# Kernel tuning notes

Measured on AMD Instinct MI355X. Metric: run time of the kernel, lower is better.

Reference implementation:

```python
import jax, jax.numpy as jnp
import numpy as np

E = 8          # num_experts
K = 2          # top_k
TEMP = 1.0     # router_temp
D = 1024       # model dim
H = 4 * D      # expert hidden dim
B, T = 2, 2048


def setup_inputs() -> dict:
    key = jax.random.key(0)
    ks = jax.random.split(key, 5)
    x = jax.random.normal(ks[0], (B, T, D), jnp.float32)
    gate_w = jax.random.normal(ks[1], (D, E), jnp.float32) * 0.02
    gate_b = jnp.zeros((E,), jnp.float32)
    w1 = jax.random.normal(ks[2], (E, D, H), jnp.float32) * 0.02
    b1 = jnp.zeros((E, H), jnp.float32)
    w2 = jax.random.normal(ks[3], (E, H, D), jnp.float32) * 0.02
    b2 = jnp.zeros((E, D), jnp.float32)
    return {"x": x, "gate_w": gate_w, "gate_b": gate_b,
            "w1": w1, "b1": b1, "w2": w2, "b2": b2}


def reference(x, gate_w, gate_b, w1, b1, w2, b2):
    b, t, d = x.shape
    xf = x.reshape(-1, d)                                    # [N, D]
    logits = xf @ gate_w + gate_b                            # [N, E]
    gates = jax.nn.softmax(logits / TEMP, axis=-1)
    topk_gates, topk_idx = jax.lax.top_k(gates, K)           # [N, K]
    topk_gates = topk_gates / (topk_gates.sum(-1, keepdims=True) + 1e-9)
    # combine weight per (token, expert): sum over k slots routed to expert e
    comb = (jax.nn.one_hot(topk_idx, E, dtype=xf.dtype)
            * topk_gates[..., None]).sum(axis=1)             # [N, E]
    out = jnp.zeros_like(xf)
    for e in range(E):  # small fixed loop over experts
        h = jax.nn.gelu(xf @ w1[e] + b1[e], approximate=False)  # exact GELU (torch default)
        out = out + comb[:, e:e + 1] * (h @ w2[e] + b2[e])
    return out.reshape(b, t, d)
```

## Files before the change

### kernel.cpp

```cpp
#include <hip/hip_runtime.h>
#include <math.h>

#define NTOK 4096
#define DIM  1024
#define HID  4096
#define NEXP 8
#define NROW 8192

typedef __bf16 bf16;
typedef __attribute__((ext_vector_type(8))) __bf16 bf16x8;
typedef __attribute__((ext_vector_type(4))) float floatx4;

__global__ void zero_k(int* __restrict__ p) {
    if (threadIdx.x < 16) p[threadIdx.x] = 0;
}

__global__ __launch_bounds__(256) void convx_k(const float* __restrict__ x,
                                               bf16* __restrict__ xb)
{
    size_t gid = (size_t)blockIdx.x * 256 + threadIdx.x;
    size_t eo = gid * 8;
    floatx4 a = *(const floatx4*)(x + eo);
    floatx4 b = *(const floatx4*)(x + eo + 4);
    bf16x8 v;
#pragma unroll
    for (int j = 0; j < 4; ++j) { v[j] = (bf16)a[j]; v[4 + j] = (bf16)b[j]; }
    *(bf16x8*)&xb[eo] = v;
}

__global__ __launch_bounds__(256) void router_k(
    const float* __restrict__ x, const float* __restrict__ gw, const float* __restrict__ gb,
    int* __restrict__ counts, int* __restrict__ tok_e, float* __restrict__ tok_g)
{
    __shared__ __align__(16) float gws[DIM * NEXP];
    int t = threadIdx.x;
#pragma unroll
    for (int i = 0; i < 8; ++i)
        *(floatx4*)&gws[(t * 8 + i) * 4] = *(const floatx4*)&gw[(t * 8 + i) * 4];
    __syncthreads();

    int gid = blockIdx.x * 256 + t;
    int wv = gid >> 6, lane = gid & 63;
    const float* xr = x + (size_t)wv * DIM;
    float acc[NEXP];
#pragma unroll
    for (int e = 0; e < NEXP; ++e) acc[e] = 0.f;
    int d0 = lane * 16;
#pragma unroll
    for (int j = 0; j < 16; ++j) {
        float xv = xr[d0 + j];
#pragma unroll
        for (int e = 0; e < NEXP; ++e) acc[e] += xv * gws[(d0 + j) * NEXP + e];
    }
#pragma unroll
    for (int off = 32; off > 0; off >>= 1) {
#pragma unroll
        for (int e = 0; e < NEXP; ++e) acc[e] += __shfl_xor(acc[e], off, 64);
    }
    if (lane == 0) {
        float lg[NEXP], m = -1e30f;
        for (int e = 0; e < NEXP; ++e) { lg[e] = acc[e] + gb[e]; m = fmaxf(m, lg[e]); }
        float p[NEXP], s = 0.f;
        for (int e = 0; e < NEXP; ++e) { p[e] = expf(lg[e] - m); s += p[e]; }
        int e0 = 0;
        for (int e = 1; e < NEXP; ++e) if (p[e] > p[e0]) e0 = e;
        int e1 = (e0 == 0) ? 1 : 0;
        for (int e = 0; e < NEXP; ++e) if (e != e0 && p[e] > p[e1]) e1 = e;
        float g0 = p[e0] / s, g1 = p[e1] / s;
        float gs = g0 + g1 + 1e-9f;
        g0 /= gs; g1 /= gs;
        tok_e[wv * 2] = e0; tok_e[wv * 2 + 1] = e1;
        tok_g[wv * 2] = g0; tok_g[wv * 2 + 1] = g1;
        atomicAdd(&counts[e0], 1);
        atomicAdd(&counts[e1], 1);
    }
}

__global__ void scan_k(const int* __restrict__ counts, int* __restrict__ base)
{
    if (threadIdx.x == 0) {
        int s = 0;
#pragma unroll
        for (int e = 0; e < NEXP; ++e) { base[e] = s; s += counts[e]; }
        base[NEXP] = s;
    }
}

__global__ __launch_bounds__(256) void scatter_k(
    const int* __restrict__ tok_e, const float* __restrict__ tok_g,
    const int* __restrict__ base, int* __restrict__ counts2,
    int* __restrict__ row_token, float* __restrict__ row_gate, int* __restrict__ tok_row)
{
    int tk = blockIdx.x * 256 + threadIdx.x;
    if (tk >= NTOK) return;
#pragma unroll
    for (int k = 0; k < 2; ++k) {
        int e = tok_e[tk * 2 + k];
        int slot = atomicAdd(&counts2[e], 1);
        int r = base[e] + slot;
        row_token[r] = tk;
        row_gate[r] = tok_g[tk * 2 + k];
        tok_row[tk * 2 + k] = r;
    }
}

__global__ __launch_bounds__(256) void transpose_k(
    const float* __restrict__ src, bf16* __restrict__ dst,
    int R, int sld, size_t soff, size_t es, size_t ed)
{
    int e = blockIdx.z;
    bf16* d = dst + (size_t)e * ed;
    __shared__ __align__(16) bf16 tile[64 * 80];
    int t = threadIdx.x;
    int r0 = blockIdx.y * 64, c0 = blockIdx.x * 64;
#pragma unroll
    for (int i = 0; i < 2; ++i) {
        int c = t + i * 256;
        int rr = c >> 3, cc = c & 7;
        size_t eo = soff + (size_t)e * es + (size_t)(r0 + rr) * sld + c0 + cc * 8;
        floatx4 a = *(const floatx4*)(src + eo);
        floatx4 b = *(const floatx4*)(src + eo + 4);
        bf16x8 v;
#pragma unroll
        for (int j = 0; j < 4; ++j) { v[j] = (bf16)a[j]; v[4 + j] = (bf16)b[j]; }
        *(bf16x8*)&tile[rr * 80 + cc * 8] = v;
    }
    __syncthreads();
#pragma unroll
    for (int i = 0; i < 2; ++i) {
        int c = t + i * 256;
        int oc = c & 63, occ = c >> 6;
        bf16x8 v;
#pragma unroll
        for (int j = 0; j < 8; ++j) v[j] = tile[(occ * 8 + j) * 80 + oc];
        *(bf16x8*)&d[(size_t)(c0 + oc) * R + r0 + occ * 8] = v;
    }
}

__global__ __launch_bounds__(256) void gemm1_k(
    const bf16* __restrict__ xb, const bf16* __restrict__ w1t, const float* __restrict__ b1,
    const int* __restrict__ counts, const int* __restrict__ base,
    const int* __restrict__ row_token, bf16* __restrict__ hbuf, int Nc, int bias_off)
{
    const int e = blockIdx.z;
    const int cnt = counts[e];
    const int rt = blockIdx.y;
    if (rt * 128 >= cnt) return;
    const int rb = base[e] + rt * 128;
    const int rend = base[e] + cnt;
    const int n0 = blockIdx.x * 128;

    __shared__ __align__(16) bf16 As[128 * 32];
    __shared__ __align__(16) bf16 Bs[128 * 32];

    const int t = threadIdx.x;
    const int c0 = t, c1 = t + 256;
    const int ar0 = c0 >> 2, ar1 = c1 >> 2;
    int rr0 = rb + ar0; if (rr0 > NROW - 1) rr0 = NROW - 1;
    int rr1 = rb + ar1; if (rr1 > NROW - 1) rr1 = NROW - 1;
    const int tok0 = row_token[rr0];
    const int tok1 = row_token[rr1];
    const bf16* ga0 = xb + (size_t)tok0 * DIM + (c0 & 3) * 8;
    const bf16* ga1 = xb + (size_t)tok1 * DIM + (c1 & 3) * 8;
    const bf16* wb = w1t + (size_t)e * Nc * DIM;
    const bf16* gb0 = wb + (size_t)(n0 + ar0) * DIM + (c0 & 3) * 8;
    const bf16* gb1 = wb + (size_t)(n0 + ar1) * DIM + (c1 & 3) * 8;

    floatx4 acc[4][4];
#pragma unroll
    for (int i = 0; i < 4; ++i)
#pragma unroll
        for (int j = 0; j < 4; ++j) acc[i][j] = floatx4{0.f, 0.f, 0.f, 0.f};

    const int wave = t >> 6, lane = t & 63;
    const int wr = (wave >> 1) * 64, wc = (wave & 1) * 64;
    const int lr = lane & 15;
    const int lk = (lane >> 4) * 8;

    for (int k0 = 0; k0 < DIM; k0 += 32) {
        bf16x8 va0 = *(const bf16x8*)(ga0 + k0);
        bf16x8 va1 = *(const bf16x8*)(ga1 + k0);
        bf16x8 vb0 = *(const bf16x8*)(gb0 + k0);
        bf16x8 vb1 = *(const bf16x8*)(gb1 + k0);
        __syncthreads();
        *(bf16x8*)&As[c0 * 8] = va0;
        *(bf16x8*)&As[c1 * 8] = va1;
        *(bf16x8*)&Bs[c0 * 8] = vb0;
        *(bf16x8*)&Bs[c1 * 8] = vb1;
        __syncthreads();
        bf16x8 af[4], bg[4];
#pragma unroll
        for (int i = 0; i < 4; ++i) af[i] = *(const bf16x8*)&As[(wr + i * 16 + lr) * 32 + lk];
#pragma unroll
        for (int i = 0; i < 4; ++i) bg[i] = *(const bf16x8*)&Bs[(wc + i * 16 + lr) * 32 + lk];
#pragma unroll
        for (int mi = 0; mi < 4; ++mi)
#pragma unroll
            for (int ni = 0; ni < 4; ++ni)
                acc[mi][ni] = __builtin_amdgcn_mfma_f32_16x16x32_bf16(af[mi], bg[ni], acc[mi][ni], 0, 0, 0);
    }

#pragma unroll
    for (int mi = 0; mi < 4; ++mi) {
#pragma unroll
        for (int r = 0; r < 4; ++r) {
            int m = wr + mi * 16 + (lane >> 4) * 4 + r;
            int gr = rb + m;
            if (gr < rend) {
#pragma unroll
                for (int ni = 0; ni < 4; ++ni) {
                    int col = n0 + wc + ni * 16 + lr;
                    float v = acc[mi][ni][r] + b1[e * HID + bias_off + col];
                    v = 0.5f * v * (1.f + erff(v * 0.70710678f));
                    hbuf[(size_t)gr * Nc + col] = (bf16)v;
                }
            }
        }
    }
}

__global__ __launch_bounds__(256) void gemm2_k(
    const bf16* __restrict__ hbuf, const bf16* __restrict__ w2t, const float* __restrict__ b2,
    const int* __restrict__ counts, const int* __restrict__ base,
    const float* __restrict__ row_gate, float* __restrict__ ybuf,
    int Kc, int first, int last)
{
    const int e = blockIdx.z;
    const int cnt = counts[e];
    const int rt = blockIdx.y;
    if (rt * 128 >= cnt) return;
    const int rb = base[e] + rt * 128;
    const int rend = base[e] + cnt;
    const int n0 = blockIdx.x * 128;

    __shared__ __align__(16) bf16 As[128 * 32];
    __shared__ __align__(16) bf16 Bs[128 * 32];

    const int t = threadIdx.x;
    const int c0 = t, c1 = t + 256;
    const int ar0 = c0 >> 2, ar1 = c1 >> 2;
    int rr0 = rb + ar0; if (rr0 > NROW - 1) rr0 = NROW - 1;
    int rr1 = rb + ar1; if (rr1 > NROW - 1) rr1 = NROW - 1;
    const bf16* ga0 = hbuf + (size_t)rr0 * Kc + (c0 & 3) * 8;
    const bf16* ga1 = hbuf + (size_t)rr1 * Kc + (c1 & 3) * 8;
    const bf16* wb = w2t + (size_t)e * DIM * Kc;
    const bf16* gb0 = wb + (size_t)(n0 + ar0) * Kc + (c0 & 3) * 8;
    const bf16* gb1 = wb + (size_t)(n0 + ar1) * Kc + (c1 & 3) * 8;

    floatx4 acc[4][4];
#pragma unroll
    for (int i = 0; i < 4; ++i)
#pragma unroll
        for (int j = 0; j < 4; ++j) acc[i][j] = floatx4{0.f, 0.f, 0.f, 0.f};

    const int wave = t >> 6, lane = t & 63;
    const int wr = (wave >> 1) * 64, wc = (wave & 1) * 64;
    const int lr = lane & 15;
    const int lk = (lane >> 4) * 8;

    for (int k0 = 0; k0 < Kc; k0 += 32) {
        bf16x8 va0 = *(const bf16x8*)(ga0 + k0);
        bf16x8 va1 = *(const bf16x8*)(ga1 + k0);
        bf16x8 vb0 = *(const bf16x8*)(gb0 + k0);
        bf16x8 vb1 = *(const bf16x8*)(gb1 + k0);
        __syncthreads();
        *(bf16x8*)&As[c0 * 8] = va0;
        *(bf16x8*)&As[c1 * 8] = va1;
        *(bf16x8*)&Bs[c0 * 8] = vb0;
        *(bf16x8*)&Bs[c1 * 8] = vb1;
        __syncthreads();
        bf16x8 af[4], bg[4];
#pragma unroll
        for (int i = 0; i < 4; ++i) af[i] = *(const bf16x8*)&As[(wr + i * 16 + lr) * 32 + lk];
#pragma unroll
        for (int i = 0; i < 4; ++i) bg[i] = *(const bf16x8*)&Bs[(wc + i * 16 + lr) * 32 + lk];
#pragma unroll
        for (int mi = 0; mi < 4; ++mi)
#pragma unroll
            for (int ni = 0; ni < 4; ++ni)
                acc[mi][ni] = __builtin_amdgcn_mfma_f32_16x16x32_bf16(af[mi], bg[ni], acc[mi][ni], 0, 0, 0);
    }

#pragma unroll
    for (int mi = 0; mi < 4; ++mi) {
#pragma unroll
        for (int r = 0; r < 4; ++r) {
            int m = wr + mi * 16 + (lane >> 4) * 4 + r;
            int gr = rb + m;
            if (gr < rend) {
#pragma unroll
                for (int ni = 0; ni < 4; ++ni) {
                    int col = n0 + wc + ni * 16 + lr;
                    size_t idx = (size_t)gr * DIM + col;
                    float v = acc[mi][ni][r];
                    if (last) {
                        float prev = first ? 0.f : ybuf[idx];
                        ybuf[idx] = row_gate[gr] * (prev + v + b2[e * DIM + col]);
                    } else {
                        ybuf[idx] = first ? v : (ybuf[idx] + v);
                    }
                }
            }
        }
    }
}

__global__ __launch_bounds__(256) void combine_k(
    const float* __restrict__ ybuf, const int* __restrict__ tok_row, float* __restrict__ out)
{
    int i = blockIdx.x * 256 + threadIdx.x;
    int tk = i >> 8;
    int dc = (i & 255) * 4;
    int ra = tok_row[tk * 2], rb = tok_row[tk * 2 + 1];
    floatx4 a = *(const floatx4*)&ybuf[(size_t)ra * DIM + dc];
    floatx4 b = *(const floatx4*)&ybuf[(size_t)rb * DIM + dc];
    floatx4 o;
#pragma unroll
    for (int j = 0; j < 4; ++j) o[j] = a[j] + b[j];
    *(floatx4*)&out[(size_t)tk * DIM + dc] = o;
}

extern "C" void kernel_launch(void* const* d_in, const int* in_sizes, int n_in,
                              void* d_out, int out_size, void* d_ws, size_t ws_size,
                              hipStream_t stream)
{
    const float* x  = (const float*)d_in[0];
    const float* gw = (const float*)d_in[1];
    const float* gb = (const float*)d_in[2];
    const float* w1 = (const float*)d_in[3];
    const float* b1 = (const float*)d_in[4];
    const float* w2 = (const float*)d_in[5];
    const float* b2 = (const float*)d_in[6];
    float* out = (float*)d_out;

    char* w = (char*)d_ws;
    int*   counts  = (int*)(w + 0);
    int*   counts2 = (int*)(w + 32);
    int*   base    = (int*)(w + 64);
    int*   tok_e   = (int*)(w + 256);
    float* tok_g   = (float*)(w + 256 + 32768);
    int*   row_tok = (int*)(w + 256 + 2 * 32768);
    float* row_g   = (float*)(w + 256 + 3 * 32768);
    int*   tok_row = (int*)(w + 256 + 4 * 32768);
    size_t off = 256 + 5 * 32768;
    bf16*  xb   = (bf16*)(w + off);   off += (size_t)NTOK * DIM * 2;
    float* ybuf = (float*)(w + off);  off += (size_t)NROW * DIM * 4;

    int Hc = HID;
    for (;;) {
        size_t need = off + (size_t)NEXP * Hc * DIM * 2 + (size_t)NROW * Hc * 2;
        if (need <= ws_size || Hc == 128) break;
        Hc >>= 1;
    }
    bf16* wT   = (bf16*)(w + off);  off += (size_t)NEXP * Hc * DIM * 2;
    bf16* hbuf = (bf16*)(w + off);

    zero_k<<<1, 64, 0, stream>>>(counts);
    router_k<<<NTOK / 4, 256, 0, stream>>>(x, gw, gb, counts, tok_e, tok_g);
    scan_k<<<1, 64, 0, stream>>>(counts, base);
    scatter_k<<<NTOK / 256, 256, 0, stream>>>(tok_e, tok_g, base, counts2, row_tok, row_g, tok_row);
    convx_k<<<(NTOK * DIM) / 2048, 256, 0, stream>>>(x, xb);

    const int nc = HID / Hc;
    for (int ch = 0; ch < nc; ++ch) {
        transpose_k<<<dim3(Hc / 64, DIM / 64, NEXP), 256, 0, stream>>>(
            w1, wT, DIM, HID, (size_t)ch * Hc, (size_t)DIM * HID, (size_t)Hc * DIM);
        gemm1_k<<<dim3(Hc / 128, 32, NEXP), 256, 0, stream>>>(
            xb, wT, b1, counts, base, row_tok, hbuf, Hc, ch * Hc);
        transpose_k<<<dim3(DIM / 64, Hc / 64, NEXP), 256, 0, stream>>>(
            w2, wT, Hc, DIM, (size_t)ch * Hc * DIM, (size_t)HID * DIM, (size_t)DIM * Hc);
        gemm2_k<<<dim3(DIM / 128, 32, NEXP), 256, 0, stream>>>(
            hbuf, wT, b2, counts, base, row_g, ybuf, Hc, ch == 0, ch == nc - 1);
    }

    combine_k<<<NTOK, 256, 0, stream>>>(ybuf, tok_row, out);
}
```

Baseline: 779.3 us.

## Use direct global-to-LDS loads with XOR-swizzled shared tiles in expert GEMMs

```diff
diff --git a/kernel.cpp b/kernel.cpp
--- a/kernel.cpp
+++ b/kernel.cpp
@@ -10,6 +10,12 @@
 typedef __bf16 bf16;
 typedef __attribute__((ext_vector_type(8))) __bf16 bf16x8;
 typedef __attribute__((ext_vector_type(4))) float floatx4;
+
+__device__ __forceinline__ void gl_lds16(const bf16* g, bf16* l) {
+    __builtin_amdgcn_global_load_lds(
+        (const __attribute__((address_space(1))) void*)g,
+        (__attribute__((address_space(3))) void*)l, 16, 0, 0);
+}
 
 __global__ void zero_k(int* __restrict__ p) {
     if (threadIdx.x < 16) p[threadIdx.x] = 0;
@@ -110,7 +116,7 @@
 {
     int e = blockIdx.z;
     bf16* d = dst + (size_t)e * ed;
-    __shared__ __align__(16) bf16 tile[64 * 80];
+    __shared__ __align__(16) bf16 tile[64 * 64];
     int t = threadIdx.x;
     int r0 = blockIdx.y * 64, c0 = blockIdx.x * 64;
 #pragma unroll
@@ -123,16 +129,21 @@
         bf16x8 v;
 #pragma unroll
         for (int j = 0; j < 4; ++j) { v[j] = (bf16)a[j]; v[4 + j] = (bf16)b[j]; }
-        *(bf16x8*)&tile[rr * 80 + cc * 8] = v;
+        *(bf16x8*)&tile[rr * 64 + ((cc ^ ((rr >> 3) & 7)) * 8)] = v;
     }
     __syncthreads();
 #pragma unroll
     for (int i = 0; i < 2; ++i) {
         int c = t + i * 256;
-        int oc = c & 63, occ = c >> 6;
+        int oc = c >> 3;
+        int occ = c & 7;
         bf16x8 v;
 #pragma unroll
-        for (int j = 0; j < 8; ++j) v[j] = tile[(occ * 8 + j) * 80 + oc];
+        for (int j = 0; j < 8; ++j) {
+            int r = occ * 8 + j;
+            int p = (oc >> 3) ^ ((r >> 3) & 7);
+            v[j] = tile[r * 64 + p * 8 + (oc & 7)];
+        }
         *(bf16x8*)&d[(size_t)(c0 + oc) * R + r0 + occ * 8] = v;
     }
 }
@@ -154,17 +165,21 @@
     __shared__ __align__(16) bf16 Bs[128 * 32];
 
     const int t = threadIdx.x;
-    const int c0 = t, c1 = t + 256;
-    const int ar0 = c0 >> 2, ar1 = c1 >> 2;
+    const int wv = t >> 6, lane = t & 63;
+    const int s0 = t, s1 = t + 256;
+    const int ar0 = s0 >> 2, ac0 = (s0 & 3) ^ ((s0 >> 3) & 3);
+    const int ar1 = s1 >> 2, ac1 = (s1 & 3) ^ ((s1 >> 3) & 3);
     int rr0 = rb + ar0; if (rr0 > NROW - 1) rr0 = NROW - 1;
     int rr1 = rb + ar1; if (rr1 > NROW - 1) rr1 = NROW - 1;
-    const int tok0 = row_token[rr0];
-    const int tok1 = row_token[rr1];
-    const bf16* ga0 = xb + (size_t)tok0 * DIM + (c0 & 3) * 8;
-    const bf16* ga1 = xb + (size_t)tok1 * DIM + (c1 & 3) * 8;
+    const bf16* ga0 = xb + (size_t)row_token[rr0] * DIM + ac0 * 8;
+    const bf16* ga1 = xb + (size_t)row_token[rr1] * DIM + ac1 * 8;
     const bf16* wb = w1t + (size_t)e * Nc * DIM;
-    const bf16* gb0 = wb + (size_t)(n0 + ar0) * DIM + (c0 & 3) * 8;
-    const bf16* gb1 = wb + (size_t)(n0 + ar1) * DIM + (c1 & 3) * 8;
+    const bf16* gb0 = wb + (size_t)(n0 + ar0) * DIM + ac0 * 8;
+    const bf16* gb1 = wb + (size_t)(n0 + ar1) * DIM + ac1 * 8;
+    bf16* lA0 = &As[wv * 512];
+    bf16* lA1 = &As[2048 + wv * 512];
+    bf16* lB0 = &Bs[wv * 512];
+    bf16* lB1 = &Bs[2048 + wv * 512];
 
     floatx4 acc[4][4];
 #pragma unroll
@@ -172,27 +187,28 @@
 #pragma unroll
         for (int j = 0; j < 4; ++j) acc[i][j] = floatx4{0.f, 0.f, 0.f, 0.f};
 
-    const int wave = t >> 6, lane = t & 63;
-    const int wr = (wave >> 1) * 64, wc = (wave & 1) * 64;
+    const int wr = (wv >> 1) * 64, wc = (wv & 1) * 64;
     const int lr = lane & 15;
-    const int lk = (lane >> 4) * 8;
+    const int ck = lane >> 4;
 
     for (int k0 = 0; k0 < DIM; k0 += 32) {
-        bf16x8 va0 = *(const bf16x8*)(ga0 + k0);
-        bf16x8 va1 = *(const bf16x8*)(ga1 + k0);
-        bf16x8 vb0 = *(const bf16x8*)(gb0 + k0);
-        bf16x8 vb1 = *(const bf16x8*)(gb1 + k0);
         __syncthreads();
-        *(bf16x8*)&As[c0 * 8] = va0;
-        *(bf16x8*)&As[c1 * 8] = va1;
-        *(bf16x8*)&Bs[c0 * 8] = vb0;
-        *(bf16x8*)&Bs[c1 * 8] = vb1;
+        gl_lds16(ga0 + k0, lA0);
+        gl_lds16(ga1 + k0, lA1);
+        gl_lds16(gb0 + k0, lB0);
+        gl_lds16(gb1 + k0, lB1);
         __syncthreads();
         bf16x8 af[4], bg[4];
 #pragma unroll
-        for (int i = 0; i < 4; ++i) af[i] = *(const bf16x8*)&As[(wr + i * 16 + lr) * 32 + lk];
-#pragma unroll
-        for (int i = 0; i < 4; ++i) bg[i] = *(const bf16x8*)&Bs[(wc + i * 16 + lr) * 32 + lk];
+        for (int i = 0; i < 4; ++i) {
+            int r = wr + i * 16 + lr;
+            af[i] = *(const bf16x8*)&As[r * 32 + ((ck ^ ((r >> 1) & 3)) * 8)];
+        }
+#pragma unroll
+        for (int i = 0; i < 4; ++i) {
+            int r = wc + i * 16 + lr;
+            bg[i] = *(const bf16x8*)&Bs[r * 32 + ((ck ^ ((r >> 1) & 3)) * 8)];
+        }
 #pragma unroll
         for (int mi = 0; mi < 4; ++mi)
 #pragma unroll
@@ -237,15 +253,21 @@
     __shared__ __align__(16) bf16 Bs[128 * 32];
 
     const int t = threadIdx.x;
-    const int c0 = t, c1 = t + 256;
-    const int ar0 = c0 >> 2, ar1 = c1 >> 2;
+    const int wv = t >> 6, lane = t & 63;
+    const int s0 = t, s1 = t + 256;
+    const int ar0 = s0 >> 2, ac0 = (s0 & 3) ^ ((s0 >> 3) & 3);
+    const int ar1 = s1 >> 2, ac1 = (s1 & 3) ^ ((s1 >> 3) & 3);
     int rr0 = rb + ar0; if (rr0 > NROW - 1) rr0 = NROW - 1;
     int rr1 = rb + ar1; if (rr1 > NROW - 1) rr1 = NROW - 1;
-    const bf16* ga0 = hbuf + (size_t)rr0 * Kc + (c0 & 3) * 8;
-    const bf16* ga1 = hbuf + (size_t)rr1 * Kc + (c1 & 3) * 8;
+    const bf16* ga0 = hbuf + (size_t)rr0 * Kc + ac0 * 8;
+    const bf16* ga1 = hbuf + (size_t)rr1 * Kc + ac1 * 8;
     const bf16* wb = w2t + (size_t)e * DIM * Kc;
-    const bf16* gb0 = wb + (size_t)(n0 + ar0) * Kc + (c0 & 3) * 8;
-    const bf16* gb1 = wb + (size_t)(n0 + ar1) * Kc + (c1 & 3) * 8;
+    const bf16* gb0 = wb + (size_t)(n0 + ar0) * Kc + ac0 * 8;
+    const bf16* gb1 = wb + (size_t)(n0 + ar1) * Kc + ac1 * 8;
+    bf16* lA0 = &As[wv * 512];
+    bf16* lA1 = &As[2048 + wv * 512];
+    bf16* lB0 = &Bs[wv * 512];
+    bf16* lB1 = &Bs[2048 + wv * 512];
 
     floatx4 acc[4][4];
 #pragma unroll
@@ -253,27 +275,28 @@
 #pragma unroll
         for (int j = 0; j < 4; ++j) acc[i][j] = floatx4{0.f, 0.f, 0.f, 0.f};
 
-    const int wave = t >> 6, lane = t & 63;
-    const int wr = (wave >> 1) * 64, wc = (wave & 1) * 64;
+    const int wr = (wv >> 1) * 64, wc = (wv & 1) * 64;
     const int lr = lane & 15;
-    const int lk = (lane >> 4) * 8;
+    const int ck = lane >> 4;
 
     for (int k0 = 0; k0 < Kc; k0 += 32) {
-        bf16x8 va0 = *(const bf16x8*)(ga0 + k0);
-        bf16x8 va1 = *(const bf16x8*)(ga1 + k0);
-        bf16x8 vb0 = *(const bf16x8*)(gb0 + k0);
-        bf16x8 vb1 = *(const bf16x8*)(gb1 + k0);
         __syncthreads();
-        *(bf16x8*)&As[c0 * 8] = va0;
-        *(bf16x8*)&As[c1 * 8] = va1;
-        *(bf16x8*)&Bs[c0 * 8] = vb0;
-        *(bf16x8*)&Bs[c1 * 8] = vb1;
+        gl_lds16(ga0 + k0, lA0);
+        gl_lds16(ga1 + k0, lA1);
+        gl_lds16(gb0 + k0, lB0);
+        gl_lds16(gb1 + k0, lB1);
         __syncthreads();
         bf16x8 af[4], bg[4];
 #pragma unroll
-        for (int i = 0; i < 4; ++i) af[i] = *(const bf16x8*)&As[(wr + i * 16 + lr) * 32 + lk];
-#pragma unroll
-        for (int i = 0; i < 4; ++i) bg[i] = *(const bf16x8*)&Bs[(wc + i * 16 + lr) * 32 + lk];
+        for (int i = 0; i < 4; ++i) {
+            int r = wr + i * 16 + lr;
+            af[i] = *(const bf16x8*)&As[r * 32 + ((ck ^ ((r >> 1) & 3)) * 8)];
+        }
+#pragma unroll
+        for (int i = 0; i < 4; ++i) {
+            int r = wc + i * 16 + lr;
+            bg[i] = *(const bf16x8*)&Bs[r * 32 + ((ck ^ ((r >> 1) & 3)) * 8)];
+        }
 #pragma unroll
         for (int mi = 0; mi < 4; ++mi)
 #pragma unroll
```

Measured after the change: 754.3 us. 3.2% less time.
